# Kernel optimization log

Hardware: AMD Instinct MI355X
Metric: run time of the kernel (lower is better)

Reference implementation:

```python
import math
import jax, jax.numpy as jnp
import numpy as np

N_HEAD = 16
LORA_SCALE = 16.0 / 8.0  # lora_alpha / r


def lora_linear(x, W, b, A, B):
    # y = x @ W^T + b + scale * (x @ A^T) @ B^T
    base = jnp.einsum('btc,oc->bto', x, W) + b
    low = jnp.einsum('btc,rc->btr', x, A)
    return base + LORA_SCALE * jnp.einsum('btr,or->bto', low, B)


def setup_inputs() -> dict:
    key = jax.random.key(0)
    ks = jax.random.split(key, 8)
    B, T, C = 2, 2048, 1024
    r = 8
    s = 0.02
    return {
        'x': jax.random.normal(ks[0], (B, T, C), jnp.float32),
        'W_attn': jax.random.normal(ks[1], (3 * C, C), jnp.float32) * s,
        'b_attn': jnp.zeros((3 * C,), jnp.float32),
        'A_attn': jax.random.normal(ks[2], (r, C), jnp.float32) * s,
        'B_attn': jax.random.normal(ks[3], (3 * C, r), jnp.float32) * s,
        'W_proj': jax.random.normal(ks[4], (C, C), jnp.float32) * s,
        'b_proj': jnp.zeros((C,), jnp.float32),
        'A_proj': jax.random.normal(ks[5], (r, C), jnp.float32) * s,
        'B_proj': jax.random.normal(ks[6], (C, r), jnp.float32) * s,
    }


def reference(x, W_attn, b_attn, A_attn, B_attn, W_proj, b_proj, A_proj, B_proj):
    B, T, C = x.shape
    H = N_HEAD
    hd = C // H
    qkv = lora_linear(x, W_attn, b_attn, A_attn, B_attn)  # [B,T,3C]
    q, k, v = jnp.split(qkv, 3, axis=2)
    # [B,H,T,hd]
    q = q.reshape(B, T, H, hd).transpose(0, 2, 1, 3)
    k = k.reshape(B, T, H, hd).transpose(0, 2, 1, 3)
    v = v.reshape(B, T, H, hd).transpose(0, 2, 1, 3)
    att = jnp.einsum('bhqd,bhkd->bhqk', q, k) * (1.0 / math.sqrt(hd))
    causal = jnp.tril(jnp.ones((T, T), bool))
    att = jnp.where(causal, att, -jnp.inf)
    att = jax.nn.softmax(att, axis=-1)
    out = jnp.einsum('bhqk,bhkd->bhqd', att, v)
    out = out.transpose(0, 2, 1, 3).reshape(B, T, C)
    return lora_linear(out, W_proj, b_proj, A_proj, B_proj)
```

## Files before the change

### kernel.cpp

```cpp
#include <hip/hip_runtime.h>
#include <hip/hip_bf16.h>
#include <stdint.h>

typedef __bf16 bf16_t;
typedef __bf16 bf16x8 __attribute__((ext_vector_type(8)));
typedef __bf16 bf16x4 __attribute__((ext_vector_type(4)));
typedef __bf16 bf16x2 __attribute__((ext_vector_type(2)));
typedef float f32x4 __attribute__((ext_vector_type(4)));
typedef float f32x16 __attribute__((ext_vector_type(16)));
typedef uint32_t u32;
typedef uint32_t u32x4 __attribute__((ext_vector_type(4)));

typedef __attribute__((address_space(1))) void as1void;
typedef __attribute__((address_space(3))) void as3void;

#define LOG2E 1.44269504088896340736f

__device__ __forceinline__ void gll16(const void* g, void* l) {
  __builtin_amdgcn_global_load_lds((as1void*)g, (as3void*)l, 16, 0, 0);
}

__device__ __forceinline__ u32 pack2(float a, float b) {
  bf16x2 t = {(bf16_t)a, (bf16_t)b};
  return __builtin_bit_cast(u32, t);
}

__global__ void prep_weff2(const float* __restrict__ W_attn, const float* __restrict__ B_attn,
                           const float* __restrict__ A_attn, const float* __restrict__ W_proj,
                           const float* __restrict__ B_proj, const float* __restrict__ A_proj,
                           bf16_t* __restrict__ WaE, bf16_t* __restrict__ WpE) {
  int idx = blockIdx.x * 256 + threadIdx.x;
  const float *W, *Bm, *Am;
  bf16_t* dst;
  if (idx < 3145728) {
    W = W_attn; Bm = B_attn; Am = A_attn; dst = WaE;
  } else {
    idx -= 3145728;
    W = W_proj; Bm = B_proj; Am = A_proj; dst = WpE;
  }
  int o = idx >> 10, c = idx & 1023;
  float acc = W[idx];
#pragma unroll
  for (int r = 0; r < 8; ++r)
    acc += 2.0f * Bm[o * 8 + r] * Am[r * 1024 + c];
  dst[idx] = (bf16_t)acc;
}

__global__ void cast_bf4(const float4* __restrict__ X, bf16x4* __restrict__ Xb, int n4) {
  int i = blockIdx.x * 256 + threadIdx.x;
  if (i < n4) {
    float4 v = X[i];
    bf16x4 o = {(bf16_t)v.x, (bf16_t)v.y, (bf16_t)v.z, (bf16_t)v.w};
    Xb[i] = o;
  }
}

template <bool QKV>
__global__ __launch_bounds__(256, 3) void gemm_bt(
    const bf16_t* __restrict__ A, const bf16_t* __restrict__ Bt,
    const float* __restrict__ bias,
    bf16_t* __restrict__ Qb, bf16_t* __restrict__ Kb, bf16_t* __restrict__ Vb,
    float* __restrict__ Out) {
  __shared__ bf16_t Als[128][64];
  __shared__ bf16_t Bls[128][64];
  const int m0 = blockIdx.x * 128;
  const int n0 = blockIdx.y * 128;
  const int tid = threadIdx.x;
  const int lane = tid & 63;
  const int w = tid >> 6;
  const int wm = w >> 1, wn = w & 1;
  const int lr = lane & 15, g = lane >> 4;
  const int sw = (lane & 7) << 3;
  const int srow = lane >> 3;
  const int soff = ((lane & 7) ^ srow) * 8;

  f32x4 acc[4][4] = {};

  for (int k0 = 0; k0 < 1024; k0 += 64) {
#pragma unroll
    for (int c = 0; c < 4; ++c) {
      int r = w * 32 + c * 8 + srow;
      gll16(A + (size_t)(m0 + r) * 1024 + k0 + soff, &Als[w * 32 + c * 8][0]);
      gll16(Bt + (size_t)(n0 + r) * 1024 + k0 + soff, &Bls[w * 32 + c * 8][0]);
    }
    __syncthreads();
#pragma unroll
    for (int ks = 0; ks < 2; ++ks) {
      bf16x8 af[4], bfv[4];
#pragma unroll
      for (int i = 0; i < 4; ++i)
        af[i] = *(const bf16x8*)&Als[wm * 64 + i * 16 + lr][(ks * 32 + g * 8) ^ sw];
#pragma unroll
      for (int j = 0; j < 4; ++j)
        bfv[j] = *(const bf16x8*)&Bls[wn * 64 + j * 16 + lr][(ks * 32 + g * 8) ^ sw];
#pragma unroll
      for (int i = 0; i < 4; ++i)
#pragma unroll
        for (int j = 0; j < 4; ++j)
          acc[i][j] = __builtin_amdgcn_mfma_f32_16x16x32_bf16(af[i], bfv[j], acc[i][j], 0, 0, 0);
    }
    __syncthreads();
  }

#pragma unroll
  for (int i = 0; i < 4; ++i) {
#pragma unroll
    for (int j = 0; j < 4; ++j) {
#pragma unroll
      for (int e = 0; e < 4; ++e) {
        int m = m0 + wm * 64 + i * 16 + g * 4 + e;
        int n = n0 + wn * 64 + j * 16 + lr;
        float v = acc[i][j][e] + bias[n];
        if (QKV) {
          int b = m >> 11, t = m & 2047;
          int which = n >> 10, hn = n & 1023;
          int h = hn >> 6, d = hn & 63;
          bf16_t* dst = (which == 0) ? Qb : (which == 1) ? Kb : Vb;
          dst[(((size_t)(b * 16 + h)) * 2048 + t) * 64 + d] = (bf16_t)v;
        } else {
          Out[(size_t)m * 1024 + n] = v;
        }
      }
    }
  }
}

__global__ __launch_bounds__(256, 2) void attn_fwd(
    const bf16_t* __restrict__ Qb, const bf16_t* __restrict__ Kb,
    const bf16_t* __restrict__ Vb, bf16_t* __restrict__ Ob) {
  __shared__ bf16_t Kls[128][64];
  __shared__ bf16_t Vt[64][128];

  int id = blockIdx.x;
  int xcd = id & 7, j = id >> 3;
  int lo = j & 31, hi2 = j >> 5;
  int bh = xcd * 4 + (lo & 3);
  int qb = hi2 ? 15 - (lo >> 2) : (lo >> 2);
  int b = bh >> 4, h = bh & 15;

  const int tid = threadIdx.x, lane = tid & 63, w = tid >> 6;
  const int q32 = lane & 31;
  const int hi = lane >> 5;
  const int ksw = (q32 & 7) << 3;
  const int vkey = ((q32 & 7) ^ (q32 >> 2)) << 3;
  const bf16_t* Qp = Qb + (size_t)bh * 2048 * 64;
  const bf16_t* Kp = Kb + (size_t)bh * 2048 * 64;
  const bf16_t* Vp = Vb + (size_t)bh * 2048 * 64;
  const float sc = 0.125f * LOG2E;

  const int q0 = qb * 128;
  const int qrow = q0 + w * 32 + q32;

  bf16x8 qf[4];
#pragma unroll
  for (int ds = 0; ds < 4; ++ds)
    qf[ds] = *(const bf16x8*)(Qp + (size_t)qrow * 64 + ds * 16 + hi * 8);

  float m_run = -3e38f, l_run = 0.f;
  f32x16 o_acc[2] = {};
  const int ktiles = qb + 1;

  for (int kt = 0; kt < ktiles; ++kt) {
    const int k0 = kt * 128;
    const bool lastt = (kt == ktiles - 1);
    const int nfa = lastt ? (w + 1) : 4;
    __syncthreads();

#pragma unroll
    for (int c = 0; c < 4; ++c) {
      int rb = w * 32 + c * 8;
      gll16(Kp + (size_t)(k0 + rb + (lane >> 3)) * 64 + ((lane & 7) ^ (lane >> 3)) * 8,
            &Kls[rb][0]);
    }

    {
      int kbase = (tid >> 4) * 8;
      int dbase = (tid & 15) * 4;
      uint2 rowv[8];
#pragma unroll
      for (int r = 0; r < 8; ++r)
        rowv[r] = *(const uint2*)(Vp + (size_t)(k0 + kbase + r) * 64 + dbase);
#pragma unroll
      for (int dd = 0; dd < 4; ++dd) {
        u32 sel = (dd & 1) ? 0x07060302u : 0x05040100u;
        u32 a0 = (dd >> 1) ? rowv[0].y : rowv[0].x;
        u32 a1 = (dd >> 1) ? rowv[1].y : rowv[1].x;
        u32 a2 = (dd >> 1) ? rowv[2].y : rowv[2].x;
        u32 a3 = (dd >> 1) ? rowv[3].y : rowv[3].x;
        u32 a4 = (dd >> 1) ? rowv[4].y : rowv[4].x;
        u32 a5 = (dd >> 1) ? rowv[5].y : rowv[5].x;
        u32 a6 = (dd >> 1) ? rowv[6].y : rowv[6].x;
        u32 a7 = (dd >> 1) ? rowv[7].y : rowv[7].x;
        int4 val;
        val.x = __builtin_amdgcn_perm(a1, a0, sel);
        val.y = __builtin_amdgcn_perm(a3, a2, sel);
        val.z = __builtin_amdgcn_perm(a5, a4, sel);
        val.w = __builtin_amdgcn_perm(a7, a6, sel);
        int d = dbase + dd;
        int key = ((d & 7) ^ ((d >> 2) & 7)) << 3;
        *(int4*)&Vt[d][kbase ^ key] = val;
      }
    }
    __syncthreads();

    f32x16 s[4] = {};
#pragma unroll
    for (int fa = 0; fa < 4; ++fa) {
      if (fa < nfa) {
#pragma unroll
        for (int ds = 0; ds < 4; ++ds) {
          bf16x8 kf = *(const bf16x8*)&Kls[fa * 32 + q32][(ds * 16 + hi * 8) ^ ksw];
          s[fa] = __builtin_amdgcn_mfma_f32_32x32x16_bf16(kf, qf[ds], s[fa], 0, 0, 0);
        }
      }
    }

    float mloc = -3e38f;
#pragma unroll
    for (int fa = 0; fa < 4; ++fa) {
      if (fa < nfa) {
#pragma unroll
        for (int r = 0; r < 16; ++r) {
          float v = s[fa][r] * sc;
          if (lastt && fa == w) {
            int km = (r & 3) + 8 * (r >> 2) + 4 * hi;
            if (km > q32) v = -3e38f;
          }
          s[fa][r] = v;
          mloc = fmaxf(mloc, v);
        }
      }
    }
    mloc = fmaxf(mloc, __shfl_xor(mloc, 32, 64));
    if (!__all(mloc <= m_run + 8.0f)) {
      float mnew = fmaxf(m_run, mloc);
      float rs = __builtin_amdgcn_exp2f(m_run - mnew);
      m_run = mnew;
      l_run *= rs;
      o_acc[0] *= rs;
      o_acc[1] *= rs;
    }

    float lsum = 0.f;
#pragma unroll
    for (int fa = 0; fa < 4; ++fa) {
      if (fa < nfa) {
        float p[16];
#pragma unroll
        for (int r = 0; r < 16; ++r) {
          p[r] = __builtin_amdgcn_exp2f(s[fa][r] - m_run);
          lsum += p[r];
        }
        u32 x0 = pack2(p[0], p[1]),   x1 = pack2(p[2], p[3]);
        u32 x2 = pack2(p[4], p[5]),   x3 = pack2(p[6], p[7]);
        u32 y0 = pack2(p[8], p[9]),   y1 = pack2(p[10], p[11]);
        u32 y2 = pack2(p[12], p[13]), y3 = pack2(p[14], p[15]);
        u32 z0 = hi ? x0 : x2;
        u32 z1 = hi ? x1 : x3;
        u32 z2 = hi ? y0 : y2;
        u32 z3 = hi ? y1 : y3;
        z0 = (u32)__shfl_xor((int)z0, 32, 64);
        z1 = (u32)__shfl_xor((int)z1, 32, 64);
        z2 = (u32)__shfl_xor((int)z2, 32, 64);
        z3 = (u32)__shfl_xor((int)z3, 32, 64);
        u32x4 pw0 = hi ? (u32x4){z0, z1, x2, x3} : (u32x4){x0, x1, z0, z1};
        u32x4 pw1 = hi ? (u32x4){z2, z3, y2, y3} : (u32x4){y0, y1, z2, z3};
        bf16x8 P0 = __builtin_bit_cast(bf16x8, pw0);
        bf16x8 P1 = __builtin_bit_cast(bf16x8, pw1);
#pragma unroll
        for (int db = 0; db < 2; ++db) {
          int d = db * 32 + q32;
          bf16x8 vf0 = *(const bf16x8*)&Vt[d][(fa * 32 + hi * 8) ^ vkey];
          o_acc[db] = __builtin_amdgcn_mfma_f32_32x32x16_bf16(vf0, P0, o_acc[db], 0, 0, 0);
          bf16x8 vf1 = *(const bf16x8*)&Vt[d][(fa * 32 + 16 + hi * 8) ^ vkey];
          o_acc[db] = __builtin_amdgcn_mfma_f32_32x32x16_bf16(vf1, P1, o_acc[db], 0, 0, 0);
        }
      }
    }
    lsum += __shfl_xor(lsum, 32, 64);
    l_run += lsum;
  }

  float inv = 1.0f / l_run;
  bf16_t* obase = Ob + ((size_t)(b * 2048 + qrow)) * 1024 + h * 64;
#pragma unroll
  for (int db = 0; db < 2; ++db) {
#pragma unroll
    for (int rg = 0; rg < 4; ++rg) {
      bf16x4 ov = {(bf16_t)(o_acc[db][rg * 4 + 0] * inv),
                   (bf16_t)(o_acc[db][rg * 4 + 1] * inv),
                   (bf16_t)(o_acc[db][rg * 4 + 2] * inv),
                   (bf16_t)(o_acc[db][rg * 4 + 3] * inv)};
      *(bf16x4*)(obase + db * 32 + rg * 8 + hi * 4) = ov;
    }
  }
}

extern "C" void kernel_launch(void* const* d_in, const int* in_sizes, int n_in,
                              void* d_out, int out_size, void* d_ws, size_t ws_size,
                              hipStream_t stream) {
  const float* x      = (const float*)d_in[0];
  const float* W_attn = (const float*)d_in[1];
  const float* b_attn = (const float*)d_in[2];
  const float* A_attn = (const float*)d_in[3];
  const float* B_attn = (const float*)d_in[4];
  const float* W_proj = (const float*)d_in[5];
  const float* b_proj = (const float*)d_in[6];
  const float* A_proj = (const float*)d_in[7];
  const float* B_proj = (const float*)d_in[8];
  float* out = (float*)d_out;

  char* ws = (char*)d_ws;
  bf16_t* WaE = (bf16_t*)(ws);
  bf16_t* WpE = (bf16_t*)(ws + 6291456);
  bf16_t* Xb  = (bf16_t*)(ws + 8388608);
  bf16_t* Qb  = (bf16_t*)(ws + 16777216);
  bf16_t* Kb  = (bf16_t*)(ws + 25165824);
  bf16_t* Vb  = (bf16_t*)(ws + 33554432);
  bf16_t* Ob  = (bf16_t*)(ws + 41943040);

  prep_weff2<<<16384, 256, 0, stream>>>(W_attn, B_attn, A_attn, W_proj, B_proj, A_proj, WaE, WpE);
  cast_bf4<<<4096, 256, 0, stream>>>((const float4*)x, (bf16x4*)Xb, 1048576);

  gemm_bt<true><<<dim3(32, 24), 256, 0, stream>>>(Xb, WaE, b_attn, Qb, Kb, Vb, nullptr);
  attn_fwd<<<512, 256, 0, stream>>>(Qb, Kb, Vb, Ob);
  gemm_bt<false><<<dim3(32, 8), 256, 0, stream>>>(Ob, WpE, b_proj, nullptr, nullptr, nullptr, out);
}
```

Measured before the change: 118.2 us.

## Double-buffer K/V tiles in attention to overlap loads with MFMA compute

The attention kernel now keeps two LDS buffers for K and transposed V. While the current tile's QK^T, softmax and PV run, it prefetches the next tile: K through async global-to-LDS loads, and V into registers that are transposed into the other buffer after the softmax step. This removes one barrier per iteration and hides global load latency behind compute. In exchange LDS use doubles to 64KB per block, which may limit occupancy under the declared 2 blocks per CU, and the prefetched V rows add register pressure.

```diff
diff --git a/kernel.cpp b/kernel.cpp
--- a/kernel.cpp
+++ b/kernel.cpp
@@ -128,8 +128,8 @@
 __global__ __launch_bounds__(256, 2) void attn_fwd(
     const bf16_t* __restrict__ Qb, const bf16_t* __restrict__ Kb,
     const bf16_t* __restrict__ Vb, bf16_t* __restrict__ Ob) {
-  __shared__ bf16_t Kls[128][64];
-  __shared__ bf16_t Vt[64][128];
+  __shared__ bf16_t Kls[2][128][64];
+  __shared__ bf16_t Vt[2][64][128];
 
   int id = blockIdx.x;
   int xcd = id & 7, j = id >> 3;
@@ -151,6 +151,11 @@
   const int q0 = qb * 128;
   const int qrow = q0 + w * 32 + q32;
 
+  const int kbase = (tid >> 4) * 8;
+  const int dbase = (tid & 15) * 4;
+  const int ksr = lane >> 3;
+  const int kso = ((lane & 7) ^ ksr) * 8;
+
   bf16x8 qf[4];
 #pragma unroll
   for (int ds = 0; ds < 4; ++ds)
@@ -160,26 +165,98 @@
   f32x16 o_acc[2] = {};
   const int ktiles = qb + 1;
 
+  {
+    uint2 rowv[8];
+#pragma unroll
+    for (int r = 0; r < 8; ++r)
+      rowv[r] = *(const uint2*)(Vp + (size_t)(kbase + r) * 64 + dbase);
+#pragma unroll
+    for (int c = 0; c < 4; ++c) {
+      int rb = w * 32 + c * 8;
+      gll16(Kp + (size_t)(rb + ksr) * 64 + kso, &Kls[0][rb][0]);
+    }
+#pragma unroll
+    for (int dd = 0; dd < 4; ++dd) {
+      u32 sel = (dd & 1) ? 0x07060302u : 0x05040100u;
+      u32 a0 = (dd >> 1) ? rowv[0].y : rowv[0].x;
+      u32 a1 = (dd >> 1) ? rowv[1].y : rowv[1].x;
+      u32 a2 = (dd >> 1) ? rowv[2].y : rowv[2].x;
+      u32 a3 = (dd >> 1) ? rowv[3].y : rowv[3].x;
+      u32 a4 = (dd >> 1) ? rowv[4].y : rowv[4].x;
+      u32 a5 = (dd >> 1) ? rowv[5].y : rowv[5].x;
+      u32 a6 = (dd >> 1) ? rowv[6].y : rowv[6].x;
+      u32 a7 = (dd >> 1) ? rowv[7].y : rowv[7].x;
+      int4 val;
+      val.x = __builtin_amdgcn_perm(a1, a0, sel);
+      val.y = __builtin_amdgcn_perm(a3, a2, sel);
+      val.z = __builtin_amdgcn_perm(a5, a4, sel);
+      val.w = __builtin_amdgcn_perm(a7, a6, sel);
+      int d = dbase + dd;
+      int key = ((d & 7) ^ ((d >> 2) & 7)) << 3;
+      *(int4*)&Vt[0][d][kbase ^ key] = val;
+    }
+    __syncthreads();
+  }
+
+  int cb = 0;
   for (int kt = 0; kt < ktiles; ++kt) {
-    const int k0 = kt * 128;
     const bool lastt = (kt == ktiles - 1);
     const int nfa = lastt ? (w + 1) : 4;
-    __syncthreads();
-
-#pragma unroll
-    for (int c = 0; c < 4; ++c) {
-      int rb = w * 32 + c * 8;
-      gll16(Kp + (size_t)(k0 + rb + (lane >> 3)) * 64 + ((lane & 7) ^ (lane >> 3)) * 8,
-            &Kls[rb][0]);
-    }
-
-    {
-      int kbase = (tid >> 4) * 8;
-      int dbase = (tid & 15) * 4;
-      uint2 rowv[8];
+    const int k0 = kt * 128;
+    const int nb = cb ^ 1;
+
+    uint2 rowv[8];
+    if (!lastt) {
+      const int kn = k0 + 128;
 #pragma unroll
       for (int r = 0; r < 8; ++r)
-        rowv[r] = *(const uint2*)(Vp + (size_t)(k0 + kbase + r) * 64 + dbase);
+        rowv[r] = *(const uint2*)(Vp + (size_t)(kn + kbase + r) * 64 + dbase);
+#pragma unroll
+      for (int c = 0; c < 4; ++c) {
+        int rb = w * 32 + c * 8;
+        gll16(Kp + (size_t)(kn + rb + ksr) * 64 + kso, &Kls[nb][rb][0]);
+      }
+    }
+
+    f32x16 s[4] = {};
+#pragma unroll
+    for (int fa = 0; fa < 4; ++fa) {
+      if (fa < nfa) {
+#pragma unroll
+        for (int ds = 0; ds < 4; ++ds) {
+          bf16x8 kf = *(const bf16x8*)&Kls[cb][fa * 32 + q32][(ds * 16 + hi * 8) ^ ksw];
+          s[fa] = __builtin_amdgcn_mfma_f32_32x32x16_bf16(kf, qf[ds], s[fa], 0, 0, 0);
+        }
+      }
+    }
+
+    float mloc = -3e38f;
+#pragma unroll
+    for (int fa = 0; fa < 4; ++fa) {
+      if (fa < nfa) {
+#pragma unroll
+        for (int r = 0; r < 16; ++r) {
+          float v = s[fa][r] * sc;
+          if (lastt && fa == w) {
+            int km = (r & 3) + 8 * (r >> 2) + 4 * hi;
+            if (km > q32) v = -3e38f;
+          }
+          s[fa][r] = v;
+          mloc = fmaxf(mloc, v);
+        }
+      }
+    }
+    mloc = fmaxf(mloc, __shfl_xor(mloc, 32, 64));
+    if (!__all(mloc <= m_run + 8.0f)) {
+      float mnew = fmaxf(m_run, mloc);
+      float rs = __builtin_amdgcn_exp2f(m_run - mnew);
+      m_run = mnew;
+      l_run *= rs;
+      o_acc[0] *= rs;
+      o_acc[1] *= rs;
+    }
+
+    if (!lastt) {
 #pragma unroll
       for (int dd = 0; dd < 4; ++dd) {
         u32 sel = (dd & 1) ? 0x07060302u : 0x05040100u;
@@ -198,47 +275,8 @@
         val.w = __builtin_amdgcn_perm(a7, a6, sel);
         int d = dbase + dd;
         int key = ((d & 7) ^ ((d >> 2) & 7)) << 3;
-        *(int4*)&Vt[d][kbase ^ key] = val;
-      }
-    }
-    __syncthreads();
-
-    f32x16 s[4] = {};
-#pragma unroll
-    for (int fa = 0; fa < 4; ++fa) {
-      if (fa < nfa) {
-#pragma unroll
-        for (int ds = 0; ds < 4; ++ds) {
-          bf16x8 kf = *(const bf16x8*)&Kls[fa * 32 + q32][(ds * 16 + hi * 8) ^ ksw];
-          s[fa] = __builtin_amdgcn_mfma_f32_32x32x16_bf16(kf, qf[ds], s[fa], 0, 0, 0);
-        }
-      }
-    }
-
-    float mloc = -3e38f;
-#pragma unroll
-    for (int fa = 0; fa < 4; ++fa) {
-      if (fa < nfa) {
-#pragma unroll
-        for (int r = 0; r < 16; ++r) {
-          float v = s[fa][r] * sc;
-          if (lastt && fa == w) {
-            int km = (r & 3) + 8 * (r >> 2) + 4 * hi;
-            if (km > q32) v = -3e38f;
-          }
-          s[fa][r] = v;
-          mloc = fmaxf(mloc, v);
-        }
-      }
-    }
-    mloc = fmaxf(mloc, __shfl_xor(mloc, 32, 64));
-    if (!__all(mloc <= m_run + 8.0f)) {
-      float mnew = fmaxf(m_run, mloc);
-      float rs = __builtin_amdgcn_exp2f(m_run - mnew);
-      m_run = mnew;
-      l_run *= rs;
-      o_acc[0] *= rs;
-      o_acc[1] *= rs;
+        *(int4*)&Vt[nb][d][kbase ^ key] = val;
+      }
     }
 
     float lsum = 0.f;
@@ -270,15 +308,18 @@
 #pragma unroll
         for (int db = 0; db < 2; ++db) {
           int d = db * 32 + q32;
-          bf16x8 vf0 = *(const bf16x8*)&Vt[d][(fa * 32 + hi * 8) ^ vkey];
+          bf16x8 vf0 = *(const bf16x8*)&Vt[cb][d][(fa * 32 + hi * 8) ^ vkey];
           o_acc[db] = __builtin_amdgcn_mfma_f32_32x32x16_bf16(vf0, P0, o_acc[db], 0, 0, 0);
-          bf16x8 vf1 = *(const bf16x8*)&Vt[d][(fa * 32 + 16 + hi * 8) ^ vkey];
+          bf16x8 vf1 = *(const bf16x8*)&Vt[cb][d][(fa * 32 + 16 + hi * 8) ^ vkey];
           o_acc[db] = __builtin_amdgcn_mfma_f32_32x32x16_bf16(vf1, P1, o_acc[db], 0, 0, 0);
         }
       }
     }
     lsum += __shfl_xor(lsum, 32, 64);
     l_run += lsum;
+
+    __syncthreads();
+    cb = nb;
   }
 
   float inv = 1.0f / l_run;
```

Measured after the change: 112.4 us. -4.9%, faster.
